# Optimization experiments

Measured on AMD Instinct MI355X. Metric: run time of the kernel, lower is better.

## Reference

```python
import jax, jax.numpy as jnp
import numpy as np
from math import sqrt

EPS = 1e-5
N_BISECT = 30

def _entmax15_impl(x):
    # alpha=1.5 entmax along last axis via bisection (entmax_bisect, alpha=1.5)
    xs = x * 0.5  # (alpha-1) * x
    mx = jnp.max(xs, axis=-1, keepdims=True)
    d = xs.shape[-1]
    lo = mx - 1.0
    hi = mx - d ** -0.5  # d^{-(alpha-1)}
    def body(i, carry):
        lo, hi = carry
        mid = 0.5 * (lo + hi)
        f = jnp.sum(jnp.square(jnp.maximum(xs - mid, 0.0)), -1, keepdims=True) - 1.0
        lo = jnp.where(f > 0, mid, lo)
        hi = jnp.where(f > 0, hi, mid)
        return lo, hi
    lo, hi = jax.lax.fori_loop(0, N_BISECT, body, (lo, hi))
    tau = 0.5 * (lo + hi)
    p = jnp.square(jnp.maximum(xs - tau, 0.0))
    return p / jnp.sum(p, -1, keepdims=True)

@jax.custom_vjp
def entmax15(x):
    return _entmax15_impl(x)

def _entmax15_fwd(x):
    p = _entmax15_impl(x)
    return p, p

def _entmax15_bwd(p, g):
    # exact entmax-1.5 backward (entmax repo): gppr = sqrt(p) on support
    s = jnp.sqrt(p)
    dx = g * s
    q = jnp.sum(dx, -1, keepdims=True) / jnp.sum(s, -1, keepdims=True)
    return (dx - q * s,)

entmax15.defvjp(_entmax15_fwd, _entmax15_bwd)

def layer_norm(x, g, b):
    m = jnp.mean(x, -1, keepdims=True)
    v = jnp.var(x, -1, keepdims=True)
    return (x - m) / jnp.sqrt(v + EPS) * g + b

def mlp(x, w1, b1, w2, b2):
    return jax.nn.gelu(x @ w1 + b1, approximate=False) @ w2 + b2

def hopfield_core(q_in, k_in, H, wq, bq, wk, bk, wv, bv, wo, bo):
    # Faithful to Hopfield.forward with mix=True; `values` arg of the torch
    # module is ignored (it recomputes value_projection(key_projection(keys))).
    B, L, _ = q_in.shape
    S = k_in.shape[1]
    q = (q_in @ wq + bq).reshape(B, L, H, -1)
    k = k_in @ wk + bk
    v = (k @ wv + bv).reshape(B, S, H, -1)
    kh = k.reshape(B, S, H, -1)
    E = q.shape[-1]
    scores = jnp.einsum('blhe,bshe->bhls', q, kh) * (1.0 / sqrt(E))
    A = entmax15(scores)
    out = jnp.einsum('bhls,bshd->blhd', A, v)
    # mix=True: transpose(2,1) then view(B, L, -1) on contiguous (B,H,L,D)
    out = jnp.transpose(out, (0, 2, 1, 3)).reshape(B, L, -1)
    return out @ wo + bo

def _forward(n_heads, x, ct_wq, ct_bq, ct_wk, ct_bk, ct_wv, ct_bv, ct_wo, ct_bo,
             cs_wq, cs_bq, cs_wk, cs_bk, cs_wv, cs_bv, cs_wo, cs_bo, cs_key,
             hp_wq, hp_bq, hp_wk, hp_bk, hp_wv, hp_bv, hp_wo, hp_bo,
             n1_g, n1_b, n2_g, n2_b, n3_g, n3_b, n4_g, n4_b,
             m1_w1, m1_b1, m1_w2, m1_b2, m2_w1, m2_b1, m2_w2, m2_b2):
    b, ts_d, seg, d = x.shape
    time_in = x.reshape(b * ts_d, seg, d)
    time_enc = hopfield_core(time_in, time_in, n_heads,
                             ct_wq, ct_bq, ct_wk, ct_bk, ct_wv, ct_bv, ct_wo, ct_bo)
    dim_in = layer_norm(time_in + time_enc, n1_g, n1_b)
    dim_in = layer_norm(dim_in + mlp(dim_in, m1_w1, m1_b1, m1_w2, m1_b2), n2_g, n2_b)
    # '(b ts_d) seg d -> (b seg) ts_d d'
    series_in = dim_in.reshape(b, ts_d, seg, d).transpose(0, 2, 1, 3).reshape(b * seg, ts_d, d)
    # HopfieldPooling: learned stored patterns as keys
    pooled_keys = jnp.broadcast_to(cs_key, (b * seg,) + cs_key.shape[1:])
    series_h = hopfield_core(series_in, pooled_keys, n_heads,
                             cs_wq, cs_bq, cs_wk, cs_bk, cs_wv, cs_bv, cs_wo, cs_bo)
    pooled_h = hopfield_core(series_in, series_in, n_heads,
                             hp_wq, hp_bq, hp_wk, hp_bk, hp_wv, hp_bv, hp_wo, hp_bo)
    dim_enc = layer_norm(series_h + pooled_h, n3_g, n3_b)
    dim_enc = layer_norm(dim_enc + mlp(dim_enc, m2_w1, m2_b1, m2_w2, m2_b2), n4_g, n4_b)
    # '(b seg) ts_d d -> b ts_d seg d'
    return dim_enc.reshape(b, seg, ts_d, d).transpose(0, 2, 1, 3)

def setup_inputs() -> dict:
    b, ts_d, seg, d, h, dff, factor = 8, 32, 64, 1024, 16, 4096, 10
    keys = iter(jax.random.split(jax.random.key(0), 64))
    def rn(shape, s=0.02):
        return jax.random.normal(next(keys), shape, jnp.float32) * s
    inp = {"x": jax.random.normal(next(keys), (b, ts_d, seg, d), jnp.float32)}
    for p in ("ct", "cs", "hp"):
        inp[p + "_wq"] = rn((d, d)); inp[p + "_bq"] = rn((d,))
        inp[p + "_wk"] = rn((d, d)); inp[p + "_bk"] = rn((d,))
        inp[p + "_wv"] = rn((d, d)); inp[p + "_bv"] = rn((d,))
        inp[p + "_wo"] = rn((d, d)); inp[p + "_bo"] = rn((d,))
    inp["cs_key"] = rn((1, factor, d), 0.1)
    for i in ("1", "2", "3", "4"):
        inp["n" + i + "_g"] = jnp.ones((d,), jnp.float32)
        inp["n" + i + "_b"] = jnp.zeros((d,), jnp.float32)
    for m in ("m1", "m2"):
        inp[m + "_w1"] = rn((d, dff)); inp[m + "_b1"] = rn((dff,))
        inp[m + "_w2"] = rn((dff, d)); inp[m + "_b2"] = rn((d,))
    inp["n_heads"] = h
    return inp

def reference(x, ct_wq, ct_bq, ct_wk, ct_bk, ct_wv, ct_bv, ct_wo, ct_bo,
              cs_wq, cs_bq, cs_wk, cs_bk, cs_wv, cs_bv, cs_wo, cs_bo, cs_key,
              hp_wq, hp_bq, hp_wk, hp_bk, hp_wv, hp_bv, hp_wo, hp_bo,
              n1_g, n1_b, n2_g, n2_b, n3_g, n3_b, n4_g, n4_b,
              m1_w1, m1_b1, m1_w2, m1_b2, m2_w1, m2_b1, m2_w2, m2_b2, n_heads):
    return _forward(n_heads, x, ct_wq, ct_bq, ct_wk, ct_bk, ct_wv, ct_bv, ct_wo, ct_bo,
                    cs_wq, cs_bq, cs_wk, cs_bk, cs_wv, cs_bv, cs_wo, cs_bo, cs_key,
                    hp_wq, hp_bq, hp_wk, hp_bk, hp_wv, hp_bv, hp_wo, hp_bo,
                    n1_g, n1_b, n2_g, n2_b, n3_g, n3_b, n4_g, n4_b,
                    m1_w1, m1_b1, m1_w2, m1_b2, m2_w1, m2_b1, m2_w2, m2_b2)
```

## Files before the change

### kernel.cpp

```cpp
#include <hip/hip_runtime.h>
#include <cstdio>

typedef __bf16 bf16x8 __attribute__((ext_vector_type(8)));
typedef float f32x4 __attribute__((ext_vector_type(4)));
typedef int i32x4 __attribute__((ext_vector_type(4)));
typedef unsigned short u16x4 __attribute__((ext_vector_type(4)));

__device__ __forceinline__ float bf2f(unsigned short u) {
  union { unsigned int i; float f; } x; x.i = ((unsigned int)u) << 16; return x.f;
}
__device__ __forceinline__ unsigned short f2bf(float f) {
  union { float f; unsigned int i; } x; x.f = f;
  unsigned int r = x.i + 0x7fffu + ((x.i >> 16) & 1u);
  return (unsigned short)(r >> 16);
}

__device__ __forceinline__ void gl2lds16(const unsigned short* g, unsigned short* l) {
  __builtin_amdgcn_global_load_lds((const __attribute__((address_space(1))) unsigned int*)g,
                                   (__attribute__((address_space(3))) unsigned int*)l, 16, 0, 0);
}

__global__ __launch_bounds__(256) void k_cast(const float* __restrict__ in,
                                              unsigned short* __restrict__ out, int n4) {
  int i = blockIdx.x * 256 + threadIdx.x;
  if (i >= n4) return;
  f32x4 v = ((const f32x4*)in)[i];
  u16x4 o;
  o[0] = f2bf(v[0]); o[1] = f2bf(v[1]); o[2] = f2bf(v[2]); o[3] = f2bf(v[3]);
  ((u16x4*)out)[i] = o;
}

__global__ __launch_bounds__(256) void k_tcast(const float* __restrict__ src,
                                               unsigned short* __restrict__ dst,
                                               int K, int N) {
  __shared__ float tile[32][33];
  int gx = blockIdx.x * 32;
  int gy = blockIdx.y * 32;
  int t = threadIdx.x;
  int c = t & 31, r0 = t >> 5;
#pragma unroll
  for (int i = 0; i < 4; i++) {
    int r = r0 + i * 8;
    tile[r][c] = src[(size_t)(gy + r) * N + gx + c];
  }
  __syncthreads();
#pragma unroll
  for (int i = 0; i < 4; i++) {
    int r = r0 + i * 8;
    dst[(size_t)(gx + r) * K + gy + c] = f2bf(tile[c][r]);
  }
}

template <bool GELU>
__global__ __launch_bounds__(256) void k_gemm(const unsigned short* __restrict__ A,
                                              const unsigned short* __restrict__ Bt,
                                              const float* __restrict__ bias,
                                              unsigned short* __restrict__ C,
                                              int M, int N, int K) {
  __shared__ unsigned short As[3][128 * 32];
  __shared__ unsigned short Bs[3][128 * 32];
  const int rowA0 = blockIdx.y * 128, colB0 = blockIdx.x * 128;
  const int t = threadIdx.x, w = t >> 6, lane = t & 63;
  const int wr = w >> 1, wc = w & 1;
  const int srow = w * 16 + (lane >> 2);
  const int schunk = (lane & 3) ^ ((lane >> 3) & 3);
  const unsigned short* pa = A + (size_t)(rowA0 + srow) * K + schunk * 8;
  const unsigned short* pb = Bt + (size_t)(colB0 + srow) * K + schunk * 8;
  const size_t row64 = (size_t)64 * K;

  f32x4 acc[4][4] = {};
  const int g = lane >> 4, ra = lane & 15;
  const int gp8 = (g ^ ((ra >> 1) & 3)) * 8;

  auto stage = [&](int buf, int kk) {
    gl2lds16(pa + kk,         &As[buf][w * 512]);
    gl2lds16(pa + row64 + kk, &As[buf][2048 + w * 512]);
    gl2lds16(pb + kk,         &Bs[buf][w * 512]);
    gl2lds16(pb + row64 + kk, &Bs[buf][2048 + w * 512]);
  };

  const int NT = K >> 5;
  stage(0, 0);
  if (NT > 1) stage(1, 32);
  int cur = 0;
  for (int j = 0; j < NT; ++j) {
    if (j + 2 < NT) {
      int nxt2 = cur + 2; if (nxt2 >= 3) nxt2 -= 3;
      stage(nxt2, (j + 2) * 32);
      asm volatile("s_waitcnt vmcnt(8)" ::: "memory");
    } else if (j + 1 < NT) {
      asm volatile("s_waitcnt vmcnt(4)" ::: "memory");
    } else {
      asm volatile("s_waitcnt vmcnt(0)" ::: "memory");
    }
    __syncthreads();
    bf16x8 af[4], bfr[4];
#pragma unroll
    for (int m = 0; m < 4; m++)
      af[m] = *(const bf16x8*)&As[cur][(wr * 64 + m * 16 + ra) * 32 + gp8];
#pragma unroll
    for (int n = 0; n < 4; n++)
      bfr[n] = *(const bf16x8*)&Bs[cur][(wc * 64 + n * 16 + ra) * 32 + gp8];
#pragma unroll
    for (int m = 0; m < 4; m++)
#pragma unroll
      for (int n = 0; n < 4; n++)
        acc[m][n] = __builtin_amdgcn_mfma_f32_16x16x32_bf16(af[m], bfr[n], acc[m][n], 0, 0, 0);
    __syncthreads();
    cur += 1; if (cur >= 3) cur -= 3;
  }

  unsigned short* Ep = &As[0][0] + w * 1024;
  const int grow0 = rowA0 + wr * 64;
  const int gcol0 = colB0 + wc * 64;
  float bv[4];
#pragma unroll
  for (int n = 0; n < 4; n++) bv[n] = bias[gcol0 + n * 16 + ra];
  const int rdrow = lane >> 3, rg = lane & 7;
#pragma unroll
  for (int m = 0; m < 4; m++) {
#pragma unroll
    for (int n = 0; n < 4; n++)
#pragma unroll
      for (int i = 0; i < 4; i++) {
        int r = g * 4 + i;
        float v = acc[m][n][i] + bv[n];
        if (GELU) v = 0.5f * v * (1.f + erff(v * 0.70710678118654752f));
        Ep[r * 64 + ((ra + n * 16) ^ ((r & 7) << 3))] = f2bf(v);
      }
    asm volatile("s_waitcnt lgkmcnt(0)" ::: "memory");
    __builtin_amdgcn_sched_barrier(0);
#pragma unroll
    for (int p = 0; p < 2; p++) {
      int rr = p * 8 + rdrow;
      bf16x8 val = *(const bf16x8*)&Ep[rr * 64 + ((rg ^ (rr & 7)) << 3)];
      *(bf16x8*)&C[(size_t)(grow0 + m * 16 + rr) * N + gcol0 + rg * 8] = val;
    }
    asm volatile("s_waitcnt lgkmcnt(0)" ::: "memory");
  }
}

__global__ __launch_bounds__(256) void k_gemm10(const unsigned short* __restrict__ A,
                                                const unsigned short* __restrict__ Bt,
                                                const float* __restrict__ bias,
                                                unsigned short* __restrict__ C) {
  __shared__ float af[1024];
  int m = blockIdx.x, nb = blockIdx.y;
  int t = threadIdx.x;
#pragma unroll
  for (int i = 0; i < 4; i++) af[t * 4 + i] = bf2f(A[(size_t)m * 1024 + t * 4 + i]);
  __syncthreads();
  int w = t >> 6, lane = t & 63;
  for (int n = nb * 64 + w; n < nb * 64 + 64; n += 4) {
    const unsigned short* brow = Bt + (size_t)n * 1024 + lane * 16;
    float acc = 0.f;
#pragma unroll
    for (int j = 0; j < 16; j++) acc += af[lane * 16 + j] * bf2f(brow[j]);
#pragma unroll
    for (int o = 32; o; o >>= 1) acc += __shfl_xor(acc, o);
    if (lane == 0) C[(size_t)m * 1024 + n] = f2bf(acc + bias[n]);
  }
}

template <int L, int S, bool SHARED>
__global__ __launch_bounds__(256) void k_attn(const unsigned short* __restrict__ Q,
                                              const unsigned short* __restrict__ Kb,
                                              const unsigned short* __restrict__ Vb,
                                              unsigned short* __restrict__ Out) {
  constexpr int SP = (S <= 32) ? 32 : 64;
  constexpr int QST = 72;
  constexpr int VST = SP + 8;
  constexpr int CST = SP + 4;
  __shared__ unsigned short Qs[L * QST];
  __shared__ unsigned short Ks[SP * QST];
  __shared__ unsigned short Vt[64 * VST];
  __shared__ float Sc[L * CST];
  __shared__ float Rps[L];
  const int blk = blockIdx.x, batch = blk >> 4, h = blk & 15;
  const int t = threadIdx.x, w = t >> 6, lane = t & 63;

  for (int c = t; c < L * 8; c += 256) {
    int r = c >> 3, ch = (c & 7) * 8;
    *(i32x4*)&Qs[r * QST + ch] =
        *(const i32x4*)&Q[((size_t)(batch * L + r)) * 1024 + h * 64 + ch];
  }
  for (int c = t; c < SP * 8; c += 256) {
    int r = c >> 3, ch = (c & 7) * 8;
    i32x4 v = {0, 0, 0, 0};
    if (r < S) {
      size_t rb = SHARED ? (size_t)r : (size_t)(batch * S + r);
      v = *(const i32x4*)&Kb[rb * 1024 + h * 64 + ch];
    }
    *(i32x4*)&Ks[r * QST + ch] = v;
  }
  for (int c = t; c < SP * 64; c += 256) {
    int s = c >> 6, e = c & 63;
    unsigned short v = 0;
    if (s < S) {
      size_t rb = SHARED ? (size_t)s : (size_t)(batch * S + s);
      v = Vb[rb * 1024 + h * 64 + e];
    }
    Vt[e * VST + s] = v;
  }
  __syncthreads();

  const int ka = (lane >> 4) * 8, ra = lane & 15;
  const int cr = (lane >> 4) * 4, cc = lane & 15;
  constexpr int NT = SP / 16, TT = (L / 16) * NT;
  for (int tt = w; tt < TT; tt += 4) {
    int m = tt / NT, n = tt % NT;
    f32x4 a = {0.f, 0.f, 0.f, 0.f};
#pragma unroll
    for (int ks = 0; ks < 2; ks++) {
      bf16x8 af = *(const bf16x8*)&Qs[(m * 16 + ra) * QST + ks * 32 + ka];
      bf16x8 bf = *(const bf16x8*)&Ks[(n * 16 + ra) * QST + ks * 32 + ka];
      a = __builtin_amdgcn_mfma_f32_16x16x32_bf16(af, bf, a, 0, 0, 0);
    }
#pragma unroll
    for (int i = 0; i < 4; i++)
      Sc[(m * 16 + cr + i) * CST + n * 16 + cc] = a[i] * 0.0625f;
  }
  __syncthreads();

  constexpr int G = 256 / L, RW = 64 / G, SL = SP / G;
  const int row = w * RW + lane / G, sub = lane % G;
  float xs[SL];
#pragma unroll
  for (int j = 0; j < SL; j++) {
    int s = sub * SL + j;
    float v = Sc[row * CST + s];
    if (S < SP && s >= S) v = -1e30f;
    xs[j] = v;
  }
  float mx = xs[0];
#pragma unroll
  for (int j = 1; j < SL; j++) mx = fmaxf(mx, xs[j]);
#pragma unroll
  for (int o = G / 2; o; o >>= 1) mx = fmaxf(mx, __shfl_xor(mx, o));
  const float hoff = (S == 64) ? 0.125f : (S == 32) ? 0.17677669529663687f : 0.31622776601683794f;
  float lo = mx - 1.f, hi = mx - hoff;
#pragma unroll 1
  for (int it = 0; it < 26; it++) {
    float mid = 0.5f * (lo + hi);
    float f = 0.f;
#pragma unroll
    for (int j = 0; j < SL; j++) { float dd = fmaxf(xs[j] - mid, 0.f); f += dd * dd; }
#pragma unroll
    for (int o = G / 2; o; o >>= 1) f += __shfl_xor(f, o);
    bool gt = f > 1.f;
    lo = gt ? mid : lo;
    hi = gt ? hi : mid;
  }
  float tau = 0.5f * (lo + hi);
  float ps = 0.f;
#pragma unroll
  for (int j = 0; j < SL; j++) { float dd = fmaxf(xs[j] - tau, 0.f); xs[j] = dd * dd; ps += xs[j]; }
#pragma unroll
  for (int o = G / 2; o; o >>= 1) ps += __shfl_xor(ps, o);
  if (sub == 0) Rps[row] = 1.f / ps;
  unsigned short* Pb = Qs;
#pragma unroll
  for (int j = 0; j < SL; j += 4) {
    u16x4 pv;
#pragma unroll
    for (int jj = 0; jj < 4; jj++) pv[jj] = f2bf(xs[j + jj]);
    *(u16x4*)&Pb[row * VST + sub * SL + j] = pv;
  }
  __syncthreads();

  constexpr int TT2 = (L / 16) * 4;
  for (int tt = w; tt < TT2; tt += 4) {
    int m = tt >> 2, n = tt & 3;
    f32x4 a = {0.f, 0.f, 0.f, 0.f};
#pragma unroll
    for (int ks = 0; ks < SP / 32; ks++) {
      bf16x8 af = *(const bf16x8*)&Pb[(m * 16 + ra) * VST + ks * 32 + ka];
      bf16x8 bf = *(const bf16x8*)&Vt[(n * 16 + ra) * VST + ks * 32 + ka];
      a = __builtin_amdgcn_mfma_f32_16x16x32_bf16(af, bf, a, 0, 0, 0);
    }
#pragma unroll
    for (int i = 0; i < 4; i++) {
      int l = m * 16 + cr + i, e = n * 16 + cc;
      float val = a[i] * Rps[l];
      int l_new = h * (L / 16) + (l >> 4);
      int cg = (l & 15) * 64 + e;
      Out[((size_t)(batch * L + l_new)) * 1024 + cg] = f2bf(val);
    }
  }
}

template <int MODE, bool F32OUT>
__global__ __launch_bounds__(256) void k_ln(const unsigned short* __restrict__ a,
                                            const unsigned short* __restrict__ b,
                                            const float* __restrict__ g,
                                            const float* __restrict__ be,
                                            void* __restrict__ outp) {
  __shared__ float red[8];
  int r = blockIdx.x, t = threadIdx.x;
  size_t base = (size_t)r * 1024 + t * 4;
  u16x4 av = *(const u16x4*)(a + base);
  u16x4 bv = *(const u16x4*)(b + base);
  float x[4];
  float s = 0.f, ss = 0.f;
#pragma unroll
  for (int i = 0; i < 4; i++) {
    x[i] = bf2f(av[i]) + bf2f(bv[i]);
    s += x[i]; ss += x[i] * x[i];
  }
#pragma unroll
  for (int o = 32; o; o >>= 1) { s += __shfl_xor(s, o); ss += __shfl_xor(ss, o); }
  int w = t >> 6;
  if ((t & 63) == 0) { red[w] = s; red[4 + w] = ss; }
  __syncthreads();
  s = red[0] + red[1] + red[2] + red[3];
  ss = red[4] + red[5] + red[6] + red[7];
  float mean = s * (1.f / 1024.f);
  float var = ss * (1.f / 1024.f) - mean * mean;
  float rstd = rsqrtf(var + 1e-5f);
  int orow;
  if (MODE == 0) orow = r;
  else if (MODE == 1) { int bi = r >> 11, rem = r & 2047; int tt = rem >> 6, sd = rem & 63; orow = (bi << 11) + sd * 32 + tt; }
  else { int bi = r >> 11, rem = r & 2047; int sd = rem >> 5, tt = rem & 31; orow = (bi << 11) + tt * 64 + sd; }
  size_t ob = (size_t)orow * 1024 + t * 4;
  if (F32OUT) {
    f32x4 y;
#pragma unroll
    for (int i = 0; i < 4; i++) y[i] = (x[i] - mean) * rstd * g[t * 4 + i] + be[t * 4 + i];
    *(f32x4*)((float*)outp + ob) = y;
  } else {
    u16x4 y;
#pragma unroll
    for (int i = 0; i < 4; i++) y[i] = f2bf((x[i] - mean) * rstd * g[t * 4 + i] + be[t * 4 + i]);
    *(u16x4*)((unsigned short*)outp + ob) = y;
  }
}


extern "C" void kernel_launch(void* const* d_in, const int* in_sizes, int n_in,
                              void* d_out, int out_size, void* d_ws, size_t ws_size,
                              hipStream_t stream) {
  const int M = 16384;
  if (n_in < 43 || in_sizes[0] != 16777216 || in_sizes[25] != 10240 || in_sizes[34] != 4194304) {
    fprintf(stderr, "kernel_launch: unexpected input layout (n_in=%d s0=%d s25=%d s34=%d)\n",
            n_in, in_sizes[0], n_in > 25 ? in_sizes[25] : -1, n_in > 34 ? in_sizes[34] : -1);
    return;
  }
  const float* x = (const float*)d_in[0];
  const float* w[3][4]; const float* bia[3][4];
  for (int p = 0; p < 3; p++) {
    w[p][0] = (const float*)d_in[1 + 8 * p + 0]; bia[p][0] = (const float*)d_in[1 + 8 * p + 1];
    w[p][1] = (const float*)d_in[1 + 8 * p + 2]; bia[p][1] = (const float*)d_in[1 + 8 * p + 3];
    w[p][2] = (const float*)d_in[1 + 8 * p + 4]; bia[p][2] = (const float*)d_in[1 + 8 * p + 5];
    w[p][3] = (const float*)d_in[1 + 8 * p + 6]; bia[p][3] = (const float*)d_in[1 + 8 * p + 7];
  }
  const float* cs_key = (const float*)d_in[25];
  const float* ng[4]; const float* nb[4];
  for (int i = 0; i < 4; i++) { ng[i] = (const float*)d_in[26 + 2 * i]; nb[i] = (const float*)d_in[27 + 2 * i]; }
  const float* m_w1[2]; const float* m_b1[2]; const float* m_w2[2]; const float* m_b2[2];
  for (int i = 0; i < 2; i++) {
    m_w1[i] = (const float*)d_in[34 + 4 * i]; m_b1[i] = (const float*)d_in[35 + 4 * i];
    m_w2[i] = (const float*)d_in[36 + 4 * i]; m_b2[i] = (const float*)d_in[37 + 4 * i];
  }

  char* base = (char*)d_ws; size_t off = 0;
  auto alloc = [&](size_t bytes) -> void* {
    off = (off + 255) & ~(size_t)255;
    void* p = base + off; off += bytes; return p;
  };
  unsigned short* Wt[3][4];
  for (int p = 0; p < 3; p++)
    for (int j = 0; j < 4; j++) Wt[p][j] = (unsigned short*)alloc((size_t)1024 * 1024 * 2);
  unsigned short* Wm1u = (unsigned short*)alloc((size_t)4096 * 1024 * 2);
  unsigned short* Wm1d = (unsigned short*)alloc((size_t)1024 * 4096 * 2);
  unsigned short* Wm2u = (unsigned short*)alloc((size_t)4096 * 1024 * 2);
  unsigned short* Wm2d = (unsigned short*)alloc((size_t)1024 * 4096 * 2);
  unsigned short* A[5];
  for (int i = 0; i < 5; i++) A[i] = (unsigned short*)alloc((size_t)M * 1024 * 2);
  unsigned short* KeyB = (unsigned short*)alloc((size_t)10 * 1024 * 2);
  unsigned short* Kcs = (unsigned short*)alloc((size_t)10 * 1024 * 2);
  unsigned short* Vcs = (unsigned short*)alloc((size_t)10 * 1024 * 2);
  if (off > ws_size) {
    fprintf(stderr, "kernel_launch: ws too small: need %zu have %zu\n", off, ws_size);
    return;
  }
  const int MC = 8192;
  unsigned short* HbT = A[0];
  unsigned short* HbS = A[1];

  auto gemm = [&](const unsigned short* Ap, const unsigned short* Bt, const float* bi,
                  unsigned short* Cp, int Mm, int Nn, int Kk, bool gelu) {
    dim3 gg(Nn / 128, Mm / 128);
    if (gelu) k_gemm<true><<<gg, 256, 0, stream>>>(Ap, Bt, bi, Cp, Mm, Nn, Kk);
    else      k_gemm<false><<<gg, 256, 0, stream>>>(Ap, Bt, bi, Cp, Mm, Nn, Kk);
  };

  for (int p = 0; p < 3; p++)
    for (int j = 0; j < 4; j++)
      k_tcast<<<dim3(32, 32), 256, 0, stream>>>(w[p][j], Wt[p][j], 1024, 1024);
  k_tcast<<<dim3(128, 32), 256, 0, stream>>>(m_w1[0], Wm1u, 1024, 4096);
  k_tcast<<<dim3(32, 128), 256, 0, stream>>>(m_w2[0], Wm1d, 4096, 1024);
  k_tcast<<<dim3(128, 32), 256, 0, stream>>>(m_w1[1], Wm2u, 1024, 4096);
  k_tcast<<<dim3(32, 128), 256, 0, stream>>>(m_w2[1], Wm2d, 4096, 1024);
  k_cast<<<16384, 256, 0, stream>>>(x, A[0], 16777216 / 4);
  k_cast<<<10, 256, 0, stream>>>(cs_key, KeyB, 10240 / 4);

  gemm(A[0], Wt[0][1], bia[0][1], A[1], M, 1024, 1024, false);
  gemm(A[0], Wt[0][0], bia[0][0], A[2], M, 1024, 1024, false);
  gemm(A[1], Wt[0][2], bia[0][2], A[3], M, 1024, 1024, false);
  k_attn<64, 64, false><<<256 * 16, 256, 0, stream>>>(A[2], A[1], A[3], A[4]);
  gemm(A[4], Wt[0][3], bia[0][3], A[1], M, 1024, 1024, false);
  k_ln<0, false><<<M, 256, 0, stream>>>(A[0], A[1], ng[0], nb[0], A[2]);
  for (int c = 0; c < M; c += MC) {
    gemm(A[2] + (size_t)c * 1024, Wm1u, m_b1[0], HbT, MC, 4096, 1024, true);
    gemm(HbT, Wm1d, m_b2[0], A[4] + (size_t)c * 1024, MC, 1024, 4096, false);
  }
  k_ln<1, false><<<M, 256, 0, stream>>>(A[2], A[4], ng[1], nb[1], A[3]);

  k_gemm10<<<dim3(10, 16), 256, 0, stream>>>(KeyB, Wt[1][1], bia[1][1], Kcs);
  k_gemm10<<<dim3(10, 16), 256, 0, stream>>>(Kcs, Wt[1][2], bia[1][2], Vcs);
  gemm(A[3], Wt[1][0], bia[1][0], A[0], M, 1024, 1024, false);
  k_attn<32, 10, true><<<512 * 16, 256, 0, stream>>>(A[0], Kcs, Vcs, A[1]);
  gemm(A[1], Wt[1][3], bia[1][3], A[2], M, 1024, 1024, false);
  gemm(A[3], Wt[2][1], bia[2][1], A[0], M, 1024, 1024, false);
  gemm(A[3], Wt[2][0], bia[2][0], A[1], M, 1024, 1024, false);
  gemm(A[0], Wt[2][2], bia[2][2], A[4], M, 1024, 1024, false);
  k_attn<32, 32, false><<<512 * 16, 256, 0, stream>>>(A[1], A[0], A[4], A[3]);
  gemm(A[3], Wt[2][3], bia[2][3], A[1], M, 1024, 1024, false);
  k_ln<0, false><<<M, 256, 0, stream>>>(A[2], A[1], ng[2], nb[2], A[0]);
  for (int c = 0; c < M; c += MC) {
    gemm(A[0] + (size_t)c * 1024, Wm2u, m_b1[1], HbS, MC, 4096, 1024, true);
    gemm(HbS, Wm2d, m_b2[1], A[3] + (size_t)c * 1024, MC, 1024, 4096, false);
  }
  k_ln<2, true><<<M, 256, 0, stream>>>(A[0], A[3], ng[3], nb[3], d_out);
}
```

Baseline: 1.759 ms.

## Enlarge GEMM tiles to 256x256 with 8 waves and grouped block swizzle

The bf16 MFMA GEMM moves from 128x128 tiles with 4 waves to 256x256 (or 128x256 for the K=4096 down-projection) tiles with 8 waves. This raises arithmetic intensity per LDS load and reduces redundant global traffic. It also adds a blockIdx swizzle that groups neighbouring workgroups for L2 reuse. The pipeline is reordered to use one barrier per k-step, issuing the next prefetch after the barrier. Larger tiles raise register pressure and LDS use and give fewer workgroups per GEMM, which may lower occupancy.

Measured after the change: 1.793 ms. No clear change (+1.9%).

```diff
diff --git a/kernel.cpp b/kernel.cpp
--- a/kernel.cpp
+++ b/kernel.cpp
@@ -51,74 +51,90 @@
   }
 }
 
-template <bool GELU>
-__global__ __launch_bounds__(256) void k_gemm(const unsigned short* __restrict__ A,
+template <int BM, bool GELU>
+__global__ __launch_bounds__(512) void k_gemm(const unsigned short* __restrict__ A,
                                               const unsigned short* __restrict__ Bt,
                                               const float* __restrict__ bias,
                                               unsigned short* __restrict__ C,
                                               int M, int N, int K) {
-  __shared__ unsigned short As[3][128 * 32];
-  __shared__ unsigned short Bs[3][128 * 32];
-  const int rowA0 = blockIdx.y * 128, colB0 = blockIdx.x * 128;
+  constexpr int RPW = BM / 2;
+  constexpr int RF = RPW / 16;
+  __shared__ unsigned short As[3][BM * 32];
+  __shared__ unsigned short Bs[3][256 * 32];
+  int nwg = gridDim.x * gridDim.y;
+  int lin = blockIdx.y * gridDim.x + blockIdx.x;
+  int swz = (nwg & 7) ? lin : ((lin & 7) * (nwg >> 3) + (lin >> 3));
+  const int rowA0 = (swz / gridDim.x) * BM, colB0 = (swz % gridDim.x) * 256;
   const int t = threadIdx.x, w = t >> 6, lane = t & 63;
-  const int wr = w >> 1, wc = w & 1;
-  const int srow = w * 16 + (lane >> 2);
-  const int schunk = (lane & 3) ^ ((lane >> 3) & 3);
-  const unsigned short* pa = A + (size_t)(rowA0 + srow) * K + schunk * 8;
-  const unsigned short* pb = Bt + (size_t)(colB0 + srow) * K + schunk * 8;
-  const size_t row64 = (size_t)64 * K;
-
-  f32x4 acc[4][4] = {};
+  const int wm = w >> 2, wn = w & 3;
   const int g = lane >> 4, ra = lane & 15;
   const int gp8 = (g ^ ((ra >> 1) & 3)) * 8;
+  const int srow = lane >> 2;
+  const int schunk = (lane & 3) ^ ((lane >> 3) & 3);
+
+  const unsigned short* paA[BM / 128];
+#pragma unroll
+  for (int i = 0; i < BM / 128; i++)
+    paA[i] = A + (size_t)(rowA0 + (w + i * 8) * 16 + srow) * K + schunk * 8;
+  const unsigned short* pbB[2];
+#pragma unroll
+  for (int i = 0; i < 2; i++)
+    pbB[i] = Bt + (size_t)(colB0 + (w + i * 8) * 16 + srow) * K + schunk * 8;
+
+  f32x4 acc[RF][4] = {};
 
   auto stage = [&](int buf, int kk) {
-    gl2lds16(pa + kk,         &As[buf][w * 512]);
-    gl2lds16(pa + row64 + kk, &As[buf][2048 + w * 512]);
-    gl2lds16(pb + kk,         &Bs[buf][w * 512]);
-    gl2lds16(pb + row64 + kk, &Bs[buf][2048 + w * 512]);
+#pragma unroll
+    for (int i = 0; i < BM / 128; i++)
+      gl2lds16(paA[i] + kk, &As[buf][(w + i * 8) * 512]);
+#pragma unroll
+    for (int i = 0; i < 2; i++)
+      gl2lds16(pbB[i] + kk, &Bs[buf][(w + i * 8) * 512]);
   };
 
   const int NT = K >> 5;
   stage(0, 0);
-  if (NT > 1) stage(1, 32);
+  stage(1, 32);
   int cur = 0;
   for (int j = 0; j < NT; ++j) {
-    if (j + 2 < NT) {
-      int nxt2 = cur + 2; if (nxt2 >= 3) nxt2 -= 3;
-      stage(nxt2, (j + 2) * 32);
-      asm volatile("s_waitcnt vmcnt(8)" ::: "memory");
-    } else if (j + 1 < NT) {
-      asm volatile("s_waitcnt vmcnt(4)" ::: "memory");
+    if (j + 1 < NT) {
+      if constexpr (BM == 256) asm volatile("s_waitcnt vmcnt(4)" ::: "memory");
+      else                     asm volatile("s_waitcnt vmcnt(3)" ::: "memory");
     } else {
       asm volatile("s_waitcnt vmcnt(0)" ::: "memory");
     }
     __syncthreads();
-    bf16x8 af[4], bfr[4];
-#pragma unroll
-    for (int m = 0; m < 4; m++)
-      af[m] = *(const bf16x8*)&As[cur][(wr * 64 + m * 16 + ra) * 32 + gp8];
+    if (j + 2 < NT) {
+      int nb = cur + 2; if (nb >= 3) nb -= 3;
+      stage(nb, (j + 2) * 32);
+    }
+    const unsigned short* Ab = &As[cur][0];
+    const unsigned short* Bb = &Bs[cur][0];
+    bf16x8 bfr[4];
 #pragma unroll
     for (int n = 0; n < 4; n++)
-      bfr[n] = *(const bf16x8*)&Bs[cur][(wc * 64 + n * 16 + ra) * 32 + gp8];
-#pragma unroll
-    for (int m = 0; m < 4; m++)
+      bfr[n] = *(const bf16x8*)&Bb[(wn * 64 + n * 16 + ra) * 32 + gp8];
+#pragma unroll
+    for (int m = 0; m < RF; m++) {
+      bf16x8 af = *(const bf16x8*)&Ab[(wm * RPW + m * 16 + ra) * 32 + gp8];
 #pragma unroll
       for (int n = 0; n < 4; n++)
-        acc[m][n] = __builtin_amdgcn_mfma_f32_16x16x32_bf16(af[m], bfr[n], acc[m][n], 0, 0, 0);
-    __syncthreads();
+        acc[m][n] = __builtin_amdgcn_mfma_f32_16x16x32_bf16(af, bfr[n], acc[m][n], 0, 0, 0);
+    }
     cur += 1; if (cur >= 3) cur -= 3;
   }
 
+  __syncthreads();
+
   unsigned short* Ep = &As[0][0] + w * 1024;
-  const int grow0 = rowA0 + wr * 64;
-  const int gcol0 = colB0 + wc * 64;
+  const int grow0 = rowA0 + wm * RPW;
+  const int gcol0 = colB0 + wn * 64;
   float bv[4];
 #pragma unroll
   for (int n = 0; n < 4; n++) bv[n] = bias[gcol0 + n * 16 + ra];
   const int rdrow = lane >> 3, rg = lane & 7;
 #pragma unroll
-  for (int m = 0; m < 4; m++) {
+  for (int m = 0; m < RF; m++) {
 #pragma unroll
     for (int n = 0; n < 4; n++)
 #pragma unroll
@@ -388,10 +404,16 @@
   unsigned short* HbS = A[1];
 
   auto gemm = [&](const unsigned short* Ap, const unsigned short* Bt, const float* bi,
-                  unsigned short* Cp, int Mm, int Nn, int Kk, bool gelu) {
-    dim3 gg(Nn / 128, Mm / 128);
-    if (gelu) k_gemm<true><<<gg, 256, 0, stream>>>(Ap, Bt, bi, Cp, Mm, Nn, Kk);
-    else      k_gemm<false><<<gg, 256, 0, stream>>>(Ap, Bt, bi, Cp, Mm, Nn, Kk);
+                  unsigned short* Cp, int Mm, int Nn, int Kk, bool gelu, bool bm128) {
+    if (bm128) {
+      dim3 gg(Nn / 256, Mm / 128);
+      if (gelu) k_gemm<128, true><<<gg, 512, 0, stream>>>(Ap, Bt, bi, Cp, Mm, Nn, Kk);
+      else      k_gemm<128, false><<<gg, 512, 0, stream>>>(Ap, Bt, bi, Cp, Mm, Nn, Kk);
+    } else {
+      dim3 gg(Nn / 256, Mm / 256);
+      if (gelu) k_gemm<256, true><<<gg, 512, 0, stream>>>(Ap, Bt, bi, Cp, Mm, Nn, Kk);
+      else      k_gemm<256, false><<<gg, 512, 0, stream>>>(Ap, Bt, bi, Cp, Mm, Nn, Kk);
+    }
   };
 
   for (int p = 0; p < 3; p++)
@@ -404,32 +426,32 @@
   k_cast<<<16384, 256, 0, stream>>>(x, A[0], 16777216 / 4);
   k_cast<<<10, 256, 0, stream>>>(cs_key, KeyB, 10240 / 4);
 
-  gemm(A[0], Wt[0][1], bia[0][1], A[1], M, 1024, 1024, false);
-  gemm(A[0], Wt[0][0], bia[0][0], A[2], M, 1024, 1024, false);
-  gemm(A[1], Wt[0][2], bia[0][2], A[3], M, 1024, 1024, false);
+  gemm(A[0], Wt[0][1], bia[0][1], A[1], M, 1024, 1024, false, false);
+  gemm(A[0], Wt[0][0], bia[0][0], A[2], M, 1024, 1024, false, false);
+  gemm(A[1], Wt[0][2], bia[0][2], A[3], M, 1024, 1024, false, false);
   k_attn<64, 64, false><<<256 * 16, 256, 0, stream>>>(A[2], A[1], A[3], A[4]);
-  gemm(A[4], Wt[0][3], bia[0][3], A[1], M, 1024, 1024, false);
+  gemm(A[4], Wt[0][3], bia[0][3], A[1], M, 1024, 1024, false, false);
   k_ln<0, false><<<M, 256, 0, stream>>>(A[0], A[1], ng[0], nb[0], A[2]);
   for (int c = 0; c < M; c += MC) {
-    gemm(A[2] + (size_t)c * 1024, Wm1u, m_b1[0], HbT, MC, 4096, 1024, true);
-    gemm(HbT, Wm1d, m_b2[0], A[4] + (size_t)c * 1024, MC, 1024, 4096, false);
+    gemm(A[2] + (size_t)c * 1024, Wm1u, m_b1[0], HbT, MC, 4096, 1024, true, false);
+    gemm(HbT, Wm1d, m_b2[0], A[4] + (size_t)c * 1024, MC, 1024, 4096, false, true);
   }
   k_ln<1, false><<<M, 256, 0, stream>>>(A[2], A[4], ng[1], nb[1], A[3]);
 
   k_gemm10<<<dim3(10, 16), 256, 0, stream>>>(KeyB, Wt[1][1], bia[1][1], Kcs);
   k_gemm10<<<dim3(10, 16), 256, 0, stream>>>(Kcs, Wt[1][2], bia[1][2], Vcs);
-  gemm(A[3], Wt[1][0], bia[1][0], A[0], M, 1024, 1024, false);
+  gemm(A[3], Wt[1][0], bia[1][0], A[0], M, 1024, 1024, false, false);
   k_attn<32, 10, true><<<512 * 16, 256, 0, stream>>>(A[0], Kcs, Vcs, A[1]);
-  gemm(A[1], Wt[1][3], bia[1][3], A[2], M, 1024, 1024, false);
-  gemm(A[3], Wt[2][1], bia[2][1], A[0], M, 1024, 1024, false);
-  gemm(A[3], Wt[2][0], bia[2][0], A[1], M, 1024, 1024, false);
-  gemm(A[0], Wt[2][2], bia[2][2], A[4], M, 1024, 1024, false);
+  gemm(A[1], Wt[1][3], bia[1][3], A[2], M, 1024, 1024, false, false);
+  gemm(A[3], Wt[2][1], bia[2][1], A[0], M, 1024, 1024, false, false);
+  gemm(A[3], Wt[2][0], bia[2][0], A[1], M, 1024, 1024, false, false);
+  gemm(A[0], Wt[2][2], bia[2][2], A[4], M, 1024, 1024, false, false);
   k_attn<32, 32, false><<<512 * 16, 256, 0, stream>>>(A[1], A[0], A[4], A[3]);
-  gemm(A[3], Wt[2][3], bia[2][3], A[1], M, 1024, 1024, false);
+  gemm(A[3], Wt[2][3], bia[2][3], A[1], M, 1024, 1024, false, false);
   k_ln<0, false><<<M, 256, 0, stream>>>(A[2], A[1], ng[2], nb[2], A[0]);
   for (int c = 0; c < M; c += MC) {
-    gemm(A[0] + (size_t)c * 1024, Wm2u, m_b1[1], HbS, MC, 4096, 1024, true);
-    gemm(HbS, Wm2d, m_b2[1], A[3] + (size_t)c * 1024, MC, 1024, 4096, false);
+    gemm(A[0] + (size_t)c * 1024, Wm2u, m_b1[1], HbS, MC, 4096, 1024, true, false);
+    gemm(HbS, Wm2d, m_b2[1], A[3] + (size_t)c * 1024, MC, 1024, 4096, false, true);
   }
   k_ln<2, true><<<M, 256, 0, stream>>>(A[0], A[3], ng[3], nb[3], d_out);
 }
```

## Fold value projection into key weights and fuse QKV into one GEMM

Applied to the files above, without the earlier changes.

The chained key-to-value projection is rewritten algebraically: Wk·Wv is precomputed with a small weight GEMM, and the folded bias bk·Wv+bv with a new kernel. Q, K and V for the cross-time and hopfield blocks then come from one N=3072 GEMM, and attention reads them through a row-stride parameter. This removes the dependent V GEMM and two launches per block, keeping the total FLOPs about the same. In exchange it adds per-call weight-folding work and some bf16 rounding error from the pre-multiplied weights.

Result: slower. 1.839 ms (+4.6%).

```diff
diff --git a/kernel.cpp b/kernel.cpp
--- a/kernel.cpp
+++ b/kernel.cpp
@@ -49,6 +49,25 @@
     int r = r0 + i * 8;
     dst[(size_t)(gx + r) * K + gy + c] = f2bf(tile[c][r]);
   }
+}
+
+__global__ __launch_bounds__(256) void k_bfold(const float* __restrict__ bk,
+                                               const float* __restrict__ wv,
+                                               const float* __restrict__ bv,
+                                               float* __restrict__ out) {
+  int n = blockIdx.x * 256 + threadIdx.x;
+  float acc = bv[n];
+#pragma unroll 8
+  for (int j = 0; j < 1024; j++) acc += bk[j] * wv[(size_t)j * 1024 + n];
+  out[n] = acc;
+}
+
+__global__ __launch_bounds__(256) void k_cpb(const float* __restrict__ a,
+                                             const float* __restrict__ b,
+                                             float* __restrict__ out) {
+  int t = blockIdx.x * 256 + threadIdx.x;
+  out[t] = a[t];
+  out[1024 + t] = b[t];
 }
 
 template <bool GELU>
@@ -115,7 +134,7 @@
   const int gcol0 = colB0 + wc * 64;
   float bv[4];
 #pragma unroll
-  for (int n = 0; n < 4; n++) bv[n] = bias[gcol0 + n * 16 + ra];
+  for (int n = 0; n < 4; n++) bv[n] = bias ? bias[gcol0 + n * 16 + ra] : 0.f;
   const int rdrow = lane >> 3, rg = lane & 7;
 #pragma unroll
   for (int m = 0; m < 4; m++) {
@@ -166,7 +185,7 @@
 __global__ __launch_bounds__(256) void k_attn(const unsigned short* __restrict__ Q,
                                               const unsigned short* __restrict__ Kb,
                                               const unsigned short* __restrict__ Vb,
-                                              unsigned short* __restrict__ Out) {
+                                              unsigned short* __restrict__ Out, int RS) {
   constexpr int SP = (S <= 32) ? 32 : 64;
   constexpr int QST = 72;
   constexpr int VST = SP + 8;
@@ -182,14 +201,14 @@
   for (int c = t; c < L * 8; c += 256) {
     int r = c >> 3, ch = (c & 7) * 8;
     *(i32x4*)&Qs[r * QST + ch] =
-        *(const i32x4*)&Q[((size_t)(batch * L + r)) * 1024 + h * 64 + ch];
+        *(const i32x4*)&Q[((size_t)(batch * L + r)) * RS + h * 64 + ch];
   }
   for (int c = t; c < SP * 8; c += 256) {
     int r = c >> 3, ch = (c & 7) * 8;
     i32x4 v = {0, 0, 0, 0};
     if (r < S) {
       size_t rb = SHARED ? (size_t)r : (size_t)(batch * S + r);
-      v = *(const i32x4*)&Kb[rb * 1024 + h * 64 + ch];
+      v = *(const i32x4*)&Kb[rb * RS + h * 64 + ch];
     }
     *(i32x4*)&Ks[r * QST + ch] = v;
   }
@@ -198,7 +217,7 @@
     unsigned short v = 0;
     if (s < S) {
       size_t rb = SHARED ? (size_t)s : (size_t)(batch * S + s);
-      v = Vb[rb * 1024 + h * 64 + e];
+      v = Vb[rb * RS + h * 64 + e];
     }
     Vt[e * VST + s] = v;
   }
@@ -341,8 +360,7 @@
                               hipStream_t stream) {
   const int M = 16384;
   if (n_in < 43 || in_sizes[0] != 16777216 || in_sizes[25] != 10240 || in_sizes[34] != 4194304) {
-    fprintf(stderr, "kernel_launch: unexpected input layout (n_in=%d s0=%d s25=%d s34=%d)\n",
-            n_in, in_sizes[0], n_in > 25 ? in_sizes[25] : -1, n_in > 34 ? in_sizes[34] : -1);
+    fprintf(stderr, "kernel_launch: unexpected input layout (n_in=%d)\n", n_in);
     return;
   }
   const float* x = (const float*)d_in[0];
@@ -367,15 +385,27 @@
     off = (off + 255) & ~(size_t)255;
     void* p = base + off; off += bytes; return p;
   };
-  unsigned short* Wt[3][4];
-  for (int p = 0; p < 3; p++)
-    for (int j = 0; j < 4; j++) Wt[p][j] = (unsigned short*)alloc((size_t)1024 * 1024 * 2);
+  const size_t W1M = (size_t)1024 * 1024;
+  unsigned short* W3ct = (unsigned short*)alloc(3 * W1M * 2);
+  unsigned short* W3hp = (unsigned short*)alloc(3 * W1M * 2);
+  unsigned short* Woct = (unsigned short*)alloc(W1M * 2);
+  unsigned short* Wohp = (unsigned short*)alloc(W1M * 2);
+  unsigned short* Wocs = (unsigned short*)alloc(W1M * 2);
+  unsigned short* Wqcs = (unsigned short*)alloc(W1M * 2);
+  unsigned short* Wkcs = (unsigned short*)alloc(W1M * 2);
+  unsigned short* Wvcs = (unsigned short*)alloc(W1M * 2);
   unsigned short* Wm1u = (unsigned short*)alloc((size_t)4096 * 1024 * 2);
   unsigned short* Wm1d = (unsigned short*)alloc((size_t)1024 * 4096 * 2);
   unsigned short* Wm2u = (unsigned short*)alloc((size_t)4096 * 1024 * 2);
   unsigned short* Wm2d = (unsigned short*)alloc((size_t)1024 * 4096 * 2);
-  unsigned short* A[5];
-  for (int i = 0; i < 5; i++) A[i] = (unsigned short*)alloc((size_t)M * 1024 * 2);
+  unsigned short* Wvt_ct = (unsigned short*)alloc(W1M * 2);
+  unsigned short* Wraw_ct = (unsigned short*)alloc(W1M * 2);
+  unsigned short* Wvt_hp = (unsigned short*)alloc(W1M * 2);
+  unsigned short* Wraw_hp = (unsigned short*)alloc(W1M * 2);
+  float* b3ct = (float*)alloc(3072 * 4);
+  float* b3hp = (float*)alloc(3072 * 4);
+  unsigned short* P[5];
+  for (int i = 0; i < 5; i++) P[i] = (unsigned short*)alloc((size_t)M * 1024 * 2);
   unsigned short* KeyB = (unsigned short*)alloc((size_t)10 * 1024 * 2);
   unsigned short* Kcs = (unsigned short*)alloc((size_t)10 * 1024 * 2);
   unsigned short* Vcs = (unsigned short*)alloc((size_t)10 * 1024 * 2);
@@ -384,8 +414,6 @@
     return;
   }
   const int MC = 8192;
-  unsigned short* HbT = A[0];
-  unsigned short* HbS = A[1];
 
   auto gemm = [&](const unsigned short* Ap, const unsigned short* Bt, const float* bi,
                   unsigned short* Cp, int Mm, int Nn, int Kk, bool gelu) {
@@ -393,43 +421,51 @@
     if (gelu) k_gemm<true><<<gg, 256, 0, stream>>>(Ap, Bt, bi, Cp, Mm, Nn, Kk);
     else      k_gemm<false><<<gg, 256, 0, stream>>>(Ap, Bt, bi, Cp, Mm, Nn, Kk);
   };
-
-  for (int p = 0; p < 3; p++)
-    for (int j = 0; j < 4; j++)
-      k_tcast<<<dim3(32, 32), 256, 0, stream>>>(w[p][j], Wt[p][j], 1024, 1024);
+  auto tc = [&](const float* src, unsigned short* dst) {
+    k_tcast<<<dim3(32, 32), 256, 0, stream>>>(src, dst, 1024, 1024);
+  };
+
+  tc(w[0][0], W3ct); tc(w[0][1], W3ct + W1M);
+  tc(w[2][0], W3hp); tc(w[2][1], W3hp + W1M);
+  tc(w[0][3], Woct); tc(w[2][3], Wohp); tc(w[1][3], Wocs);
+  tc(w[1][0], Wqcs); tc(w[1][1], Wkcs); tc(w[1][2], Wvcs);
   k_tcast<<<dim3(128, 32), 256, 0, stream>>>(m_w1[0], Wm1u, 1024, 4096);
   k_tcast<<<dim3(32, 128), 256, 0, stream>>>(m_w2[0], Wm1d, 4096, 1024);
   k_tcast<<<dim3(128, 32), 256, 0, stream>>>(m_w1[1], Wm2u, 1024, 4096);
   k_tcast<<<dim3(32, 128), 256, 0, stream>>>(m_w2[1], Wm2d, 4096, 1024);
-  k_cast<<<16384, 256, 0, stream>>>(x, A[0], 16777216 / 4);
+  tc(w[0][2], Wvt_ct); k_cast<<<1024, 256, 0, stream>>>(w[0][1], Wraw_ct, 262144);
+  tc(w[2][2], Wvt_hp); k_cast<<<1024, 256, 0, stream>>>(w[2][1], Wraw_hp, 262144);
+  k_cast<<<16384, 256, 0, stream>>>(x, P[0], 16777216 / 4);
   k_cast<<<10, 256, 0, stream>>>(cs_key, KeyB, 10240 / 4);
-
-  gemm(A[0], Wt[0][1], bia[0][1], A[1], M, 1024, 1024, false);
-  gemm(A[0], Wt[0][0], bia[0][0], A[2], M, 1024, 1024, false);
-  gemm(A[1], Wt[0][2], bia[0][2], A[3], M, 1024, 1024, false);
-  k_attn<64, 64, false><<<256 * 16, 256, 0, stream>>>(A[2], A[1], A[3], A[4]);
-  gemm(A[4], Wt[0][3], bia[0][3], A[1], M, 1024, 1024, false);
-  k_ln<0, false><<<M, 256, 0, stream>>>(A[0], A[1], ng[0], nb[0], A[2]);
+  gemm(Wvt_ct, Wraw_ct, nullptr, W3ct + 2 * W1M, 1024, 1024, 1024, false);
+  gemm(Wvt_hp, Wraw_hp, nullptr, W3hp + 2 * W1M, 1024, 1024, 1024, false);
+  k_cpb<<<4, 256, 0, stream>>>(bia[0][0], bia[0][1], b3ct);
+  k_bfold<<<4, 256, 0, stream>>>(bia[0][1], w[0][2], bia[0][2], b3ct + 2048);
+  k_cpb<<<4, 256, 0, stream>>>(bia[2][0], bia[2][1], b3hp);
+  k_bfold<<<4, 256, 0, stream>>>(bia[2][1], w[2][2], bia[2][2], b3hp + 2048);
+  k_gemm10<<<dim3(10, 16), 256, 0, stream>>>(KeyB, Wkcs, bia[1][1], Kcs);
+  k_gemm10<<<dim3(10, 16), 256, 0, stream>>>(Kcs, Wvcs, bia[1][2], Vcs);
+
+  gemm(P[0], W3ct, b3ct, P[1], M, 3072, 1024, false);
+  k_attn<64, 64, false><<<256 * 16, 256, 0, stream>>>(P[1], P[1] + 1024, P[1] + 2048, P[4], 3072);
+  gemm(P[4], Woct, bia[0][3], P[1], M, 1024, 1024, false);
+  k_ln<0, false><<<M, 256, 0, stream>>>(P[0], P[1], ng[0], nb[0], P[2]);
   for (int c = 0; c < M; c += MC) {
-    gemm(A[2] + (size_t)c * 1024, Wm1u, m_b1[0], HbT, MC, 4096, 1024, true);
-    gemm(HbT, Wm1d, m_b2[0], A[4] + (size_t)c * 1024, MC, 1024, 4096, false);
-  }
-  k_ln<1, false><<<M, 256, 0, stream>>>(A[2], A[4], ng[1], nb[1], A[3]);
-
-  k_gemm10<<<dim3(10, 16), 256, 0, stream>>>(KeyB, Wt[1][1], bia[1][1], Kcs);
-  k_gemm10<<<dim3(10, 16), 256, 0, stream>>>(Kcs, Wt[1][2], bia[1][2], Vcs);
-  gemm(A[3], Wt[1][0], bia[1][0], A[0], M, 1024, 1024, false);
-  k_attn<32, 10, true><<<512 * 16, 256, 0, stream>>>(A[0], Kcs, Vcs, A[1]);
-  gemm(A[1], Wt[1][3], bia[1][3], A[2], M, 1024, 1024, false);
-  gemm(A[3], Wt[2][1], bia[2][1], A[0], M, 1024, 1024, false);
-  gemm(A[3], Wt[2][0], bia[2][0], A[1], M, 1024, 1024, false);
-  gemm(A[0], Wt[2][2], bia[2][2], A[4], M, 1024, 1024, false);
-  k_attn<32, 32, false><<<512 * 16, 256, 0, stream>>>(A[1], A[0], A[4], A[3]);
-  gemm(A[3], Wt[2][3], bia[2][3], A[1], M, 1024, 1024, false);
-  k_ln<0, false><<<M, 256, 0, stream>>>(A[2], A[1], ng[2], nb[2], A[0]);
+    gemm(P[2] + (size_t)c * 1024, Wm1u, m_b1[0], P[3], MC, 4096, 1024, true);
+    gemm(P[3], Wm1d, m_b2[0], P[1] + (size_t)c * 1024, MC, 1024, 4096, false);
+  }
+  k_ln<1, false><<<M, 256, 0, stream>>>(P[2], P[1], ng[1], nb[1], P[3]);
+
+  gemm(P[3], W3hp, b3hp, P[0], M, 3072, 1024, false);
+  k_attn<32, 32, false><<<512 * 16, 256, 0, stream>>>(P[0], P[0] + 1024, P[0] + 2048, P[4], 3072);
+  gemm(P[4], Wohp, bia[2][3], P[1], M, 1024, 1024, false);
+  gemm(P[3], Wqcs, bia[1][0], P[2], M, 1024, 1024, false);
+  k_attn<32, 10, true><<<512 * 16, 256, 0, stream>>>(P[2], Kcs, Vcs, P[0], 1024);
+  gemm(P[0], Wocs, bia[1][3], P[2], M, 1024, 1024, false);
+  k_ln<0, false><<<M, 256, 0, stream>>>(P[2], P[1], ng[2], nb[2], P[0]);
   for (int c = 0; c < M; c += MC) {
-    gemm(A[0] + (size_t)c * 1024, Wm2u, m_b1[1], HbS, MC, 4096, 1024, true);
-    gemm(HbS, Wm2d, m_b2[1], A[3] + (size_t)c * 1024, MC, 1024, 4096, false);
-  }
-  k_ln<2, true><<<M, 256, 0, stream>>>(A[0], A[3], ng[3], nb[3], d_out);
-}
+    gemm(P[0] + (size_t)c * 1024, Wm2u, m_b1[1], P[2], MC, 4096, 1024, true);
+    gemm(P[2], Wm2d, m_b2[1], P[1] + (size_t)c * 1024, MC, 1024, 4096, false);
+  }
+  k_ln<2, true><<<M, 256, 0, stream>>>(P[0], P[1], ng[3], nb[3], d_out);
+}
```
